# Performance work log

Hardware: AMD Instinct MI355X
Metric: run time of the kernel (lower is better)

Reference implementation:

```python
import jax, jax.numpy as jnp
import numpy as np

RES = 1024
NUM_ROOMS = 8
N_AGENTS = 5_000_000


def setup_inputs() -> dict:
    key = jax.random.key(0)
    k1, k2, k3 = jax.random.split(key, 3)
    agent_positions = jax.random.uniform(k1, (N_AGENTS, 2), dtype=jnp.float32)
    room_params = jax.random.uniform(k2, (NUM_ROOMS, 4), dtype=jnp.float32)
    # torch init: params[:, 2:] = params[:, 2:] * 0.1 + 0.05  (room sigmas)
    room_params = room_params.at[:, 2:].set(room_params[:, 2:] * 0.1 + 0.05)
    wall_density = jax.random.uniform(k3, (RES, RES), dtype=jnp.float32)
    return {
        "agent_positions": agent_positions,
        "room_params": room_params,
        "wall_density": wall_density,
    }


def reference(agent_positions, room_params, wall_density):
    res = wall_density.shape[0]
    lin = jnp.linspace(0.0, 1.0, res, dtype=wall_density.dtype)
    x_grid, y_grid = jnp.meshgrid(lin, lin, indexing="ij")  # [res,res]

    # Per-room Gaussian density maps, vectorized over rooms -> [R,res,res]
    cx = room_params[:, 0, None, None]
    cy = room_params[:, 1, None, None]
    sx = room_params[:, 2, None, None]
    sy = room_params[:, 3, None, None]
    spatial_layout = jnp.exp(
        -((x_grid - cx) ** 2 / (2.0 * sx**2) + (y_grid - cy) ** 2 / (2.0 * sy**2))
    )

    # Agent flow histogram via single fused scatter-add
    ix = jnp.clip((agent_positions[:, 0] * res).astype(jnp.int32), 0, res - 1)
    iy = jnp.clip((agent_positions[:, 1] * res).astype(jnp.int32), 0, res - 1)
    flow_field = jnp.zeros((res, res), dtype=wall_density.dtype).at[ix, iy].add(1.0)
    flow_field = flow_field / (flow_field.max() + 1e-6)

    dynamic_layout = spatial_layout * (1.0 - wall_density[None, :, :])
    return (dynamic_layout, flow_field)
```

## Files before the change

kernel.cpp:

```cpp
#include <hip/hip_runtime.h>

#define RES 1024
#define NROOMS 8
#define NBUCKETS 256
#define BINS_PER_BUCKET (4 * RES)
#define CAP 32768
#define SWPB 8
#define NBLK 512
#define F4PT 10
#define STG_MAX (512 * F4PT * 2)

typedef unsigned int u32x4 __attribute__((ext_vector_type(4)));
typedef float        f32x4 __attribute__((ext_vector_type(4)));

__device__ __forceinline__ void dyn_cell(
    const float* __restrict__ room_params,
    const float4* __restrict__ wall,
    float4* __restrict__ dyn, int idx)
{
    int i  = idx >> 8;
    int j0 = (idx & 255) << 2;
    const float inv1023 = 1.0f / 1023.0f;
    float x  = (float)i * inv1023;
    float y0 = (float)(j0 + 0) * inv1023;
    float y1 = (float)(j0 + 1) * inv1023;
    float y2 = (float)(j0 + 2) * inv1023;
    float y3 = (float)(j0 + 3) * inv1023;

    float4 w = wall[idx];
    float omx = 1.0f - w.x;
    float omy = 1.0f - w.y;
    float omz = 1.0f - w.z;
    float omw = 1.0f - w.w;

    const int plane4 = (RES * RES) / 4;
    #pragma unroll
    for (int r = 0; r < NROOMS; ++r) {
        float cx = room_params[4 * r + 0];
        float cy = room_params[4 * r + 1];
        float sx = room_params[4 * r + 2];
        float sy = room_params[4 * r + 3];
        float isx = 1.0f / (2.0f * sx * sx);
        float isy = 1.0f / (2.0f * sy * sy);
        float dx = x - cx;
        float ax = dx * dx * isx;
        float d0 = y0 - cy, d1 = y1 - cy, d2 = y2 - cy, d3 = y3 - cy;
        f32x4 d;
        d.x = __expf(-(ax + d0 * d0 * isy)) * omx;
        d.y = __expf(-(ax + d1 * d1 * isy)) * omy;
        d.z = __expf(-(ax + d2 * d2 * isy)) * omz;
        d.w = __expf(-(ax + d3 * d3 * isy)) * omw;
        __builtin_nontemporal_store(
            d, reinterpret_cast<f32x4*>(&dyn[(size_t)r * plane4 + idx]));
    }
}

__global__ __launch_bounds__(512, 4) void scatter_kernel(
    const float4* __restrict__ pos, int n4, int nagents,
    unsigned short* __restrict__ buf, unsigned int* __restrict__ cursor,
    const float* __restrict__ room_params,
    const float4* __restrict__ wall,
    float4* __restrict__ dyn)
{
    __shared__ unsigned int   cnt[SWPB][NBUCKETS];
    __shared__ unsigned int   sbase[SWPB][NBUCKETS];
    __shared__ unsigned int   pstart[NBUCKETS];
    __shared__ unsigned int   ptotal[NBUCKETS];
    __shared__ unsigned int   gbase[NBUCKETS];
    __shared__ unsigned int   wsum[4];
    __shared__ unsigned short staged[STG_MAX];

    int tid  = threadIdx.x;
    int wv   = tid >> 6;
    int lane = tid & 63;

    dyn_cell(room_params, wall, dyn, blockIdx.x * 512 + tid);

    #pragma unroll
    for (int i = 0; i < (SWPB * NBUCKETS) / 512; ++i)
        ((unsigned int*)cnt)[tid + 512 * i] = 0u;
    __syncthreads();

    int chunk = (n4 + NBLK - 1) / NBLK;
    int start = blockIdx.x * chunk;
    int end   = min(start + chunk, n4);

    unsigned int   code[2 * F4PT];
    unsigned short rank[2 * F4PT];
    #pragma unroll
    for (int k = 0; k < F4PT; ++k) {
        int i4 = start + (k << 9) + tid;
        if (i4 < end) {
            f32x4 pv = __builtin_nontemporal_load(
                reinterpret_cast<const f32x4*>(&pos[i4]));
            int ix0 = min(max((int)(pv.x * 1024.0f), 0), 1023);
            int iy0 = min(max((int)(pv.y * 1024.0f), 0), 1023);
            int ix1 = min(max((int)(pv.z * 1024.0f), 0), 1023);
            int iy1 = min(max((int)(pv.w * 1024.0f), 0), 1023);
            unsigned int b0 = (unsigned int)(ix0 >> 2);
            unsigned int b1 = (unsigned int)(ix1 >> 2);
            code[2 * k]     = (b0 << 16) | (unsigned int)(((ix0 & 3) << 10) | iy0);
            code[2 * k + 1] = (b1 << 16) | (unsigned int)(((ix1 & 3) << 10) | iy1);
            rank[2 * k]     = (unsigned short)atomicAdd(&cnt[wv][b0], 1u);
            rank[2 * k + 1] = (unsigned short)atomicAdd(&cnt[wv][b1], 1u);
        } else {
            code[2 * k] = 0xFFFFFFFFu;
            code[2 * k + 1] = 0xFFFFFFFFu;
        }
    }
    __syncthreads();

    if (tid < NBUCKETS) {
        unsigned int run = 0;
        #pragma unroll
        for (int w = 0; w < SWPB; ++w) {
            unsigned int c = cnt[w][tid];
            sbase[w][tid] = run;
            run += c;
        }
        ptotal[tid] = run;
        gbase[tid]  = run ? atomicAdd(&cursor[tid], run) : 0u;
        unsigned int t = run;
        #pragma unroll
        for (int off = 1; off < 64; off <<= 1) {
            unsigned int v = (unsigned int)__shfl_up((int)t, off, 64);
            if (lane >= off) t += v;
        }
        if (lane == 63) wsum[wv] = t;
        pstart[tid] = t - run;
    }
    __syncthreads();
    if (tid < NBUCKETS) {
        unsigned int off = 0;
        #pragma unroll
        for (int w = 0; w < 3; ++w) if (w < wv) off += wsum[w];
        unsigned int ps = pstart[tid] + off;
        pstart[tid] = ps;
        #pragma unroll
        for (int w = 0; w < SWPB; ++w) sbase[w][tid] += ps;
    }
    __syncthreads();

    #pragma unroll
    for (int k = 0; k < 2 * F4PT; ++k) {
        unsigned int cd = code[k];
        if (cd != 0xFFFFFFFFu) {
            unsigned int b = cd >> 16;
            staged[sbase[wv][b] + rank[k]] = (unsigned short)(cd & 0xFFFFu);
        }
    }
    __syncthreads();

    #pragma unroll 4
    for (int bb = 0; bb < 32; ++bb) {
        int b = (wv << 5) + bb;
        unsigned int n  = ptotal[b];
        unsigned int ps = pstart[b];
        unsigned int gb = gbase[b];
        for (unsigned int e = lane; e < n; e += 64) {
            unsigned int p = gb + e;
            if (p < CAP) buf[b * CAP + p] = staged[ps + e];
        }
    }

    if (blockIdx.x == 0 && tid == 0 && (nagents & 1)) {
        const float* t = (const float*)pos;
        float px = t[2 * (nagents - 1)];
        float py = t[2 * (nagents - 1) + 1];
        int ix = min(max((int)(px * 1024.0f), 0), 1023);
        int iy = min(max((int)(py * 1024.0f), 0), 1023);
        unsigned int b = (unsigned int)(ix >> 2);
        unsigned int p = atomicAdd(&cursor[b], 1u);
        if (p < CAP) buf[b * CAP + p] = (unsigned short)(((ix & 3) << 10) | iy);
    }
}

__global__ __launch_bounds__(1024) void hist_build_kernel(
    const unsigned short* __restrict__ buf,
    const unsigned int* __restrict__ cursor,
    unsigned int* __restrict__ counts,
    unsigned int* __restrict__ out_max)
{
    __shared__ __align__(16) unsigned int h[BINS_PER_BUCKET];
    int b = blockIdx.x, tid = threadIdx.x;
    #pragma unroll
    for (int i = 0; i < BINS_PER_BUCKET / 1024; ++i) h[tid + 1024 * i] = 0u;
    __syncthreads();

    unsigned int n = min(cursor[b], (unsigned int)CAP);
    const unsigned short* seg = buf + (size_t)b * CAP;
    unsigned int n2 = n & ~1u;
    for (unsigned int i = 2 * tid; i < n2; i += 2048) {
        unsigned int u = *(const unsigned int*)(seg + i);
        atomicAdd(&h[u & 0xFFFFu], 1u);
        atomicAdd(&h[u >> 16], 1u);
    }
    if (tid == 0 && (n & 1)) atomicAdd(&h[seg[n - 1]], 1u);
    __syncthreads();

    u32x4 v = ((const u32x4*)h)[tid];
    ((u32x4*)counts)[(size_t)b * (BINS_PER_BUCKET / 4) + tid] = v;
    unsigned int m = max(max(v.x, v.y), max(v.z, v.w));
    #pragma unroll
    for (int off = 32; off > 0; off >>= 1)
        m = max(m, (unsigned int)__shfl_down((int)m, off, 64));
    __shared__ unsigned int sm[16];
    if ((tid & 63) == 0) sm[tid >> 6] = m;
    __syncthreads();
    if (tid == 0) {
        #pragma unroll
        for (int w = 1; w < 16; ++w) m = max(m, sm[w]);
        atomicMax(out_max, m);
    }
}

__global__ __launch_bounds__(256) void norm_kernel(
    float* __restrict__ flow, const unsigned int* __restrict__ maxp)
{
    int idx = blockIdx.x * blockDim.x + threadIdx.x;
    uint4 c = ((const uint4*)flow)[idx];
    float inv = 1.0f / ((float)(*maxp) + 1e-6f);
    ((float4*)flow)[idx] = make_float4((float)c.x * inv, (float)c.y * inv,
                                       (float)c.z * inv, (float)c.w * inv);
}

__global__ __launch_bounds__(256) void hist_atomic_kernel(
    const float4* __restrict__ pos, int n4, int nagents,
    unsigned int* __restrict__ counts)
{
    int idx = blockIdx.x * blockDim.x + threadIdx.x;
    int stride = gridDim.x * blockDim.x;
    for (int i = idx; i < n4; i += stride) {
        float4 p = pos[i];
        int ix0 = min(max((int)(p.x * 1024.0f), 0), 1023);
        int iy0 = min(max((int)(p.y * 1024.0f), 0), 1023);
        int ix1 = min(max((int)(p.z * 1024.0f), 0), 1023);
        int iy1 = min(max((int)(p.w * 1024.0f), 0), 1023);
        atomicAdd(&counts[(ix0 << 10) + iy0], 1u);
        atomicAdd(&counts[(ix1 << 10) + iy1], 1u);
    }
    if (idx == 0 && (nagents & 1)) {
        const float* t = (const float*)pos;
        int ix = min(max((int)(t[2 * (nagents - 1)] * 1024.0f), 0), 1023);
        int iy = min(max((int)(t[2 * (nagents - 1) + 1] * 1024.0f), 0), 1023);
        atomicAdd(&counts[(ix << 10) + iy], 1u);
    }
}

__global__ __launch_bounds__(256) void max_kernel(
    const uint4* __restrict__ counts, unsigned int* __restrict__ out_max)
{
    int idx = blockIdx.x * blockDim.x + threadIdx.x;
    int stride = gridDim.x * blockDim.x;
    unsigned int m = 0;
    const int n4 = (RES * RES) / 4;
    for (int i = idx; i < n4; i += stride) {
        uint4 c = counts[i];
        m = max(m, max(max(c.x, c.y), max(c.z, c.w)));
    }
    #pragma unroll
    for (int off = 32; off > 0; off >>= 1)
        m = max(m, (unsigned int)__shfl_down((int)m, off, 64));
    __shared__ unsigned int sm[4];
    if ((threadIdx.x & 63) == 0) sm[threadIdx.x >> 6] = m;
    __syncthreads();
    if (threadIdx.x == 0) {
        m = max(max(sm[0], sm[1]), max(sm[2], sm[3]));
        atomicMax(out_max, m);
    }
}

__global__ __launch_bounds__(256) void final_full_kernel(
    const float* __restrict__ room_params,
    const float4* __restrict__ wall,
    float4* __restrict__ dyn,
    float* __restrict__ flow,
    const unsigned int* __restrict__ maxp)
{
    int idx = blockIdx.x * blockDim.x + threadIdx.x;
    uint4 c = ((const uint4*)flow)[idx];
    float inv = 1.0f / ((float)(*maxp) + 1e-6f);
    ((float4*)flow)[idx] = make_float4((float)c.x * inv, (float)c.y * inv,
                                       (float)c.z * inv, (float)c.w * inv);
    dyn_cell(room_params, wall, dyn, idx);
}

extern "C" void kernel_launch(void* const* d_in, const int* in_sizes, int n_in,
                              void* d_out, int out_size, void* d_ws, size_t ws_size,
                              hipStream_t stream) {
    const float* agents      = (const float*)d_in[0];
    const float* room_params = (const float*)d_in[1];
    const float* wall        = (const float*)d_in[2];

    float* dyn  = (float*)d_out;
    float* flow = (float*)d_out + (size_t)NROOMS * RES * RES;
    unsigned int* counts = (unsigned int*)flow;

    int nagents = in_sizes[0] / 2;
    int n4 = nagents / 2;

    size_t need = 2048 + (size_t)NBUCKETS * CAP * sizeof(unsigned short);

    bool fits = ((n4 + NBLK - 1) / NBLK) <= (F4PT * 512);

    if (ws_size >= need && fits) {
        unsigned int*   cursor = (unsigned int*)d_ws;
        unsigned int*   maxp   = (unsigned int*)((char*)d_ws + 1024);
        unsigned short* buf    = (unsigned short*)((char*)d_ws + 2048);

        (void)hipMemsetAsync(d_ws, 0, 2048, stream);
        scatter_kernel<<<NBLK, 512, 0, stream>>>(
            (const float4*)agents, n4, nagents, buf, cursor,
            room_params, (const float4*)wall, (float4*)dyn);
        hist_build_kernel<<<NBUCKETS, 1024, 0, stream>>>(buf, cursor, counts, maxp);
        norm_kernel<<<(RES * RES / 4) / 256, 256, 0, stream>>>(flow, maxp);
    } else {
        unsigned int* maxp = (unsigned int*)d_ws;
        (void)hipMemsetAsync(flow, 0, (size_t)RES * RES * sizeof(float), stream);
        (void)hipMemsetAsync(maxp, 0, sizeof(unsigned int), stream);
        hist_atomic_kernel<<<1280, 256, 0, stream>>>((const float4*)agents, n4, nagents, counts);
        max_kernel<<<256, 256, 0, stream>>>((const uint4*)counts, maxp);
        final_full_kernel<<<(RES * RES / 4) / 256, 256, 0, stream>>>(
            room_params, (const float4*)wall, (float4*)dyn, flow, maxp);
    }
}
```

Before: 126.2 us.

## Replace bucketed two-pass histogram with direct global atomics fused with density maps

Drops the bucket-sort scatter into a workspace buffer and the shared-memory per-bucket histogram pass. Each thread now does global atomicAdd straight into the count grid, using 1024 blocks of 256 threads, and the same kernel also computes the per-room dynamic layout. A separate max kernel and a normalize kernel follow. This gives up locality in shared memory for heavily contended scattered global atomics, plus an extra memset and an extra pass over the counts.

```diff
diff --git a/kernel.cpp b/kernel.cpp
--- a/kernel.cpp
+++ b/kernel.cpp
@@ -2,16 +2,8 @@
 
 #define RES 1024
 #define NROOMS 8
-#define NBUCKETS 256
-#define BINS_PER_BUCKET (4 * RES)
-#define CAP 32768
-#define SWPB 8
-#define NBLK 512
-#define F4PT 10
-#define STG_MAX (512 * F4PT * 2)
 
-typedef unsigned int u32x4 __attribute__((ext_vector_type(4)));
-typedef float        f32x4 __attribute__((ext_vector_type(4)));
+typedef float f32x4 __attribute__((ext_vector_type(4)));
 
 __device__ __forceinline__ void dyn_cell(
     const float* __restrict__ room_params,
@@ -55,181 +47,19 @@
     }
 }
 
-__global__ __launch_bounds__(512, 4) void scatter_kernel(
+__global__ __launch_bounds__(256) void hist_atomic_dyn_kernel(
     const float4* __restrict__ pos, int n4, int nagents,
-    unsigned short* __restrict__ buf, unsigned int* __restrict__ cursor,
+    unsigned int* __restrict__ counts,
+    unsigned int* __restrict__ maxp,
     const float* __restrict__ room_params,
     const float4* __restrict__ wall,
     float4* __restrict__ dyn)
 {
-    __shared__ unsigned int   cnt[SWPB][NBUCKETS];
-    __shared__ unsigned int   sbase[SWPB][NBUCKETS];
-    __shared__ unsigned int   pstart[NBUCKETS];
-    __shared__ unsigned int   ptotal[NBUCKETS];
-    __shared__ unsigned int   gbase[NBUCKETS];
-    __shared__ unsigned int   wsum[4];
-    __shared__ unsigned short staged[STG_MAX];
+    int idx = blockIdx.x * 256 + threadIdx.x;
+    int stride = gridDim.x * 256;
 
-    int tid  = threadIdx.x;
-    int wv   = tid >> 6;
-    int lane = tid & 63;
+    if (idx == 0) *maxp = 0u;
 
-    dyn_cell(room_params, wall, dyn, blockIdx.x * 512 + tid);
-
-    #pragma unroll
-    for (int i = 0; i < (SWPB * NBUCKETS) / 512; ++i)
-        ((unsigned int*)cnt)[tid + 512 * i] = 0u;
-    __syncthreads();
-
-    int chunk = (n4 + NBLK - 1) / NBLK;
-    int start = blockIdx.x * chunk;
-    int end   = min(start + chunk, n4);
-
-    unsigned int   code[2 * F4PT];
-    unsigned short rank[2 * F4PT];
-    #pragma unroll
-    for (int k = 0; k < F4PT; ++k) {
-        int i4 = start + (k << 9) + tid;
-        if (i4 < end) {
-            f32x4 pv = __builtin_nontemporal_load(
-                reinterpret_cast<const f32x4*>(&pos[i4]));
-            int ix0 = min(max((int)(pv.x * 1024.0f), 0), 1023);
-            int iy0 = min(max((int)(pv.y * 1024.0f), 0), 1023);
-            int ix1 = min(max((int)(pv.z * 1024.0f), 0), 1023);
-            int iy1 = min(max((int)(pv.w * 1024.0f), 0), 1023);
-            unsigned int b0 = (unsigned int)(ix0 >> 2);
-            unsigned int b1 = (unsigned int)(ix1 >> 2);
-            code[2 * k]     = (b0 << 16) | (unsigned int)(((ix0 & 3) << 10) | iy0);
-            code[2 * k + 1] = (b1 << 16) | (unsigned int)(((ix1 & 3) << 10) | iy1);
-            rank[2 * k]     = (unsigned short)atomicAdd(&cnt[wv][b0], 1u);
-            rank[2 * k + 1] = (unsigned short)atomicAdd(&cnt[wv][b1], 1u);
-        } else {
-            code[2 * k] = 0xFFFFFFFFu;
-            code[2 * k + 1] = 0xFFFFFFFFu;
-        }
-    }
-    __syncthreads();
-
-    if (tid < NBUCKETS) {
-        unsigned int run = 0;
-        #pragma unroll
-        for (int w = 0; w < SWPB; ++w) {
-            unsigned int c = cnt[w][tid];
-            sbase[w][tid] = run;
-            run += c;
-        }
-        ptotal[tid] = run;
-        gbase[tid]  = run ? atomicAdd(&cursor[tid], run) : 0u;
-        unsigned int t = run;
-        #pragma unroll
-        for (int off = 1; off < 64; off <<= 1) {
-            unsigned int v = (unsigned int)__shfl_up((int)t, off, 64);
-            if (lane >= off) t += v;
-        }
-        if (lane == 63) wsum[wv] = t;
-        pstart[tid] = t - run;
-    }
-    __syncthreads();
-    if (tid < NBUCKETS) {
-        unsigned int off = 0;
-        #pragma unroll
-        for (int w = 0; w < 3; ++w) if (w < wv) off += wsum[w];
-        unsigned int ps = pstart[tid] + off;
-        pstart[tid] = ps;
-        #pragma unroll
-        for (int w = 0; w < SWPB; ++w) sbase[w][tid] += ps;
-    }
-    __syncthreads();
-
-    #pragma unroll
-    for (int k = 0; k < 2 * F4PT; ++k) {
-        unsigned int cd = code[k];
-        if (cd != 0xFFFFFFFFu) {
-            unsigned int b = cd >> 16;
-            staged[sbase[wv][b] + rank[k]] = (unsigned short)(cd & 0xFFFFu);
-        }
-    }
-    __syncthreads();
-
-    #pragma unroll 4
-    for (int bb = 0; bb < 32; ++bb) {
-        int b = (wv << 5) + bb;
-        unsigned int n  = ptotal[b];
-        unsigned int ps = pstart[b];
-        unsigned int gb = gbase[b];
-        for (unsigned int e = lane; e < n; e += 64) {
-            unsigned int p = gb + e;
-            if (p < CAP) buf[b * CAP + p] = staged[ps + e];
-        }
-    }
-
-    if (blockIdx.x == 0 && tid == 0 && (nagents & 1)) {
-        const float* t = (const float*)pos;
-        float px = t[2 * (nagents - 1)];
-        float py = t[2 * (nagents - 1) + 1];
-        int ix = min(max((int)(px * 1024.0f), 0), 1023);
-        int iy = min(max((int)(py * 1024.0f), 0), 1023);
-        unsigned int b = (unsigned int)(ix >> 2);
-        unsigned int p = atomicAdd(&cursor[b], 1u);
-        if (p < CAP) buf[b * CAP + p] = (unsigned short)(((ix & 3) << 10) | iy);
-    }
-}
-
-__global__ __launch_bounds__(1024) void hist_build_kernel(
-    const unsigned short* __restrict__ buf,
-    const unsigned int* __restrict__ cursor,
-    unsigned int* __restrict__ counts,
-    unsigned int* __restrict__ out_max)
-{
-    __shared__ __align__(16) unsigned int h[BINS_PER_BUCKET];
-    int b = blockIdx.x, tid = threadIdx.x;
-    #pragma unroll
-    for (int i = 0; i < BINS_PER_BUCKET / 1024; ++i) h[tid + 1024 * i] = 0u;
-    __syncthreads();
-
-    unsigned int n = min(cursor[b], (unsigned int)CAP);
-    const unsigned short* seg = buf + (size_t)b * CAP;
-    unsigned int n2 = n & ~1u;
-    for (unsigned int i = 2 * tid; i < n2; i += 2048) {
-        unsigned int u = *(const unsigned int*)(seg + i);
-        atomicAdd(&h[u & 0xFFFFu], 1u);
-        atomicAdd(&h[u >> 16], 1u);
-    }
-    if (tid == 0 && (n & 1)) atomicAdd(&h[seg[n - 1]], 1u);
-    __syncthreads();
-
-    u32x4 v = ((const u32x4*)h)[tid];
-    ((u32x4*)counts)[(size_t)b * (BINS_PER_BUCKET / 4) + tid] = v;
-    unsigned int m = max(max(v.x, v.y), max(v.z, v.w));
-    #pragma unroll
-    for (int off = 32; off > 0; off >>= 1)
-        m = max(m, (unsigned int)__shfl_down((int)m, off, 64));
-    __shared__ unsigned int sm[16];
-    if ((tid & 63) == 0) sm[tid >> 6] = m;
-    __syncthreads();
-    if (tid == 0) {
-        #pragma unroll
-        for (int w = 1; w < 16; ++w) m = max(m, sm[w]);
-        atomicMax(out_max, m);
-    }
-}
-
-__global__ __launch_bounds__(256) void norm_kernel(
-    float* __restrict__ flow, const unsigned int* __restrict__ maxp)
-{
-    int idx = blockIdx.x * blockDim.x + threadIdx.x;
-    uint4 c = ((const uint4*)flow)[idx];
-    float inv = 1.0f / ((float)(*maxp) + 1e-6f);
-    ((float4*)flow)[idx] = make_float4((float)c.x * inv, (float)c.y * inv,
-                                       (float)c.z * inv, (float)c.w * inv);
-}
-
-__global__ __launch_bounds__(256) void hist_atomic_kernel(
-    const float4* __restrict__ pos, int n4, int nagents,
-    unsigned int* __restrict__ counts)
-{
-    int idx = blockIdx.x * blockDim.x + threadIdx.x;
-    int stride = gridDim.x * blockDim.x;
     for (int i = idx; i < n4; i += stride) {
         float4 p = pos[i];
         int ix0 = min(max((int)(p.x * 1024.0f), 0), 1023);
@@ -245,6 +75,8 @@
         int iy = min(max((int)(t[2 * (nagents - 1) + 1] * 1024.0f), 0), 1023);
         atomicAdd(&counts[(ix << 10) + iy], 1u);
     }
+
+    dyn_cell(room_params, wall, dyn, idx);
 }
 
 __global__ __launch_bounds__(256) void max_kernel(
@@ -270,19 +102,14 @@
     }
 }
 
-__global__ __launch_bounds__(256) void final_full_kernel(
-    const float* __restrict__ room_params,
-    const float4* __restrict__ wall,
-    float4* __restrict__ dyn,
-    float* __restrict__ flow,
-    const unsigned int* __restrict__ maxp)
+__global__ __launch_bounds__(256) void norm_kernel(
+    float* __restrict__ flow, const unsigned int* __restrict__ maxp)
 {
     int idx = blockIdx.x * blockDim.x + threadIdx.x;
     uint4 c = ((const uint4*)flow)[idx];
     float inv = 1.0f / ((float)(*maxp) + 1e-6f);
     ((float4*)flow)[idx] = make_float4((float)c.x * inv, (float)c.y * inv,
                                        (float)c.z * inv, (float)c.w * inv);
-    dyn_cell(room_params, wall, dyn, idx);
 }
 
 extern "C" void kernel_launch(void* const* d_in, const int* in_sizes, int n_in,
@@ -295,32 +122,18 @@
     float* dyn  = (float*)d_out;
     float* flow = (float*)d_out + (size_t)NROOMS * RES * RES;
     unsigned int* counts = (unsigned int*)flow;
+    unsigned int* maxp   = (unsigned int*)d_ws;
 
     int nagents = in_sizes[0] / 2;
     int n4 = nagents / 2;
 
-    size_t need = 2048 + (size_t)NBUCKETS * CAP * sizeof(unsigned short);
+    (void)hipMemsetAsync(flow, 0, (size_t)RES * RES * sizeof(float), stream);
 
-    bool fits = ((n4 + NBLK - 1) / NBLK) <= (F4PT * 512);
+    hist_atomic_dyn_kernel<<<(RES * RES / 4) / 256, 256, 0, stream>>>(
+        (const float4*)agents, n4, nagents, counts, maxp,
+        room_params, (const float4*)wall, (float4*)dyn);
 
-    if (ws_size >= need && fits) {
-        unsigned int*   cursor = (unsigned int*)d_ws;
-        unsigned int*   maxp   = (unsigned int*)((char*)d_ws + 1024);
-        unsigned short* buf    = (unsigned short*)((char*)d_ws + 2048);
+    max_kernel<<<256, 256, 0, stream>>>((const uint4*)counts, maxp);
 
-        (void)hipMemsetAsync(d_ws, 0, 2048, stream);
-        scatter_kernel<<<NBLK, 512, 0, stream>>>(
-            (const float4*)agents, n4, nagents, buf, cursor,
-            room_params, (const float4*)wall, (float4*)dyn);
-        hist_build_kernel<<<NBUCKETS, 1024, 0, stream>>>(buf, cursor, counts, maxp);
-        norm_kernel<<<(RES * RES / 4) / 256, 256, 0, stream>>>(flow, maxp);
-    } else {
-        unsigned int* maxp = (unsigned int*)d_ws;
-        (void)hipMemsetAsync(flow, 0, (size_t)RES * RES * sizeof(float), stream);
-        (void)hipMemsetAsync(maxp, 0, sizeof(unsigned int), stream);
-        hist_atomic_kernel<<<1280, 256, 0, stream>>>((const float4*)agents, n4, nagents, counts);
-        max_kernel<<<256, 256, 0, stream>>>((const uint4*)counts, maxp);
-        final_full_kernel<<<(RES * RES / 4) / 256, 256, 0, stream>>>(
-            room_params, (const float4*)wall, (float4*)dyn, flow, maxp);
-    }
+    norm_kernel<<<(RES * RES / 4) / 256, 256, 0, stream>>>(flow, maxp);
 }
```

Measured after the change: 279.0 us. 121% more time.
